# Performance work log

Measured on AMD Instinct MI355X. Metric: run time of the kernel, lower is better.

Reference implementation:

```python
import jax, jax.numpy as jnp
import numpy as np

B, H, W = 8, 64, 64
EMBED, HEADS, HEAD_DIM = 768, 12, 64
FF = 3072
WS = 14  # window size
SCALE = HEAD_DIM ** -0.5
EPS = 1e-6


def setup_inputs() -> dict:
    key = jax.random.key(0)
    ks = jax.random.split(key, 8)
    def n(k, shp, s=0.02):
        return jax.random.normal(k, shp, jnp.float32) * s
    return {
        "x": jax.random.normal(ks[0], (B, H, W, EMBED), jnp.float32),
        "g1": jnp.ones((EMBED,), jnp.float32),
        "beta1": jnp.zeros((EMBED,), jnp.float32),
        "w_qkv": n(ks[1], (EMBED, 3 * EMBED)),
        "b_qkv": jnp.zeros((3 * EMBED,), jnp.float32),
        "w_proj": n(ks[2], (EMBED, EMBED)),
        "b_proj": jnp.zeros((EMBED,), jnp.float32),
        "rel_pos_h": n(ks[3], (2 * WS - 1, HEAD_DIM)),
        "rel_pos_w": n(ks[4], (2 * WS - 1, HEAD_DIM)),
        "g2": jnp.ones((EMBED,), jnp.float32),
        "beta2": jnp.zeros((EMBED,), jnp.float32),
        "w_fc1": n(ks[5], (EMBED, FF)),
        "b_fc1": jnp.zeros((FF,), jnp.float32),
        "w_fc2": n(ks[6], (FF, EMBED)),
        "b_fc2": jnp.zeros((EMBED,), jnp.float32),
    }


def layer_norm(x, g, b):
    m = jnp.mean(x, axis=-1, keepdims=True)
    v = jnp.mean(jnp.square(x - m), axis=-1, keepdims=True)
    return (x - m) * jax.lax.rsqrt(v + EPS) * g + b


def window_partition(x):
    b, h, w, c = x.shape
    ph, pw = (-h) % WS, (-w) % WS
    x = jnp.pad(x, ((0, 0), (0, ph), (0, pw), (0, 0)))
    hp, wp = h + ph, w + pw
    x = x.reshape(b, hp // WS, WS, wp // WS, WS, c)
    x = x.transpose(0, 1, 3, 2, 4, 5).reshape(-1, WS, WS, c)
    return x, (hp, wp)


def window_unpartition(win, pad_hw, hw):
    hp, wp = pad_hw
    h, w = hw
    b = win.shape[0] // ((hp // WS) * (wp // WS))
    x = win.reshape(b, hp // WS, wp // WS, WS, WS, -1)
    x = x.transpose(0, 1, 3, 2, 4, 5).reshape(b, hp, wp, -1)
    return x[:, :h, :w, :]


def attention(xw, w_qkv, b_qkv, w_proj, b_proj, rel_pos_h, rel_pos_w):
    bw, hs, ws_, c = xw.shape
    n = hs * ws_
    qkv = (xw.reshape(bw, n, c) @ w_qkv + b_qkv).reshape(bw, n, 3, HEADS, HEAD_DIM)
    q, k, v = jnp.moveaxis(qkv, 2, 0)            # each (bw, n, heads, hd)
    q = q.transpose(0, 2, 1, 3)                  # (bw, heads, n, hd)
    k = k.transpose(0, 2, 1, 3)
    v = v.transpose(0, 2, 1, 3)
    attn = jnp.einsum('bhnd,bhmd->bhnm', q * SCALE, k)
    # decomposed relative position bias (q unscaled, per torch reference)
    idx = jnp.arange(WS)[:, None] - jnp.arange(WS)[None, :] + (WS - 1)
    Rh = rel_pos_h[idx]                          # (ws, ws, hd)
    Rw = rel_pos_w[idx]
    r_q = q.reshape(bw, HEADS, WS, WS, HEAD_DIM)
    rel_h = jnp.einsum('bhpqd,pkd->bhpqk', r_q, Rh)
    rel_w = jnp.einsum('bhpqd,qkd->bhpqk', r_q, Rw)
    attn = attn.reshape(bw, HEADS, WS, WS, WS, WS)
    attn = attn + rel_h[..., :, None] + rel_w[..., None, :]
    attn = jax.nn.softmax(attn.reshape(bw, HEADS, n, n), axis=-1)
    out = jnp.einsum('bhnm,bhmd->bhnd', attn, v)
    out = out.transpose(0, 2, 1, 3).reshape(bw, hs, ws_, c)
    return out @ w_proj + b_proj


def reference(x, g1, beta1, w_qkv, b_qkv, w_proj, b_proj, rel_pos_h, rel_pos_w,
              g2, beta2, w_fc1, b_fc1, w_fc2, b_fc2):
    shortcut = x
    h = layer_norm(x, g1, beta1)
    win, pad_hw = window_partition(h)
    a = attention(win, w_qkv, b_qkv, w_proj, b_proj, rel_pos_h, rel_pos_w)
    a = window_unpartition(a, pad_hw, (x.shape[1], x.shape[2]))
    x = shortcut + a
    h2 = layer_norm(x, g2, beta2)
    mlp = jax.nn.gelu(h2 @ w_fc1 + b_fc1, approximate=False) @ w_fc2 + b_fc2
    return x + mlp
```

## Files before the change

kernel.cpp:

```cpp
#include <hip/hip_runtime.h>
#include <cstdint>


typedef unsigned short u16;
typedef __attribute__((ext_vector_type(8))) short short8;
typedef __attribute__((ext_vector_type(4))) float f32x4;

__device__ __forceinline__ u16 f2b(float f) {
    union { float f; unsigned int i; } x; x.f = f;
    unsigned int u = x.i;
    return (u16)((u + 0x7fffu + ((u >> 16) & 1u)) >> 16);
}
__device__ __forceinline__ float b2f(u16 u) {
    union { unsigned int i; float f; } x; x.i = ((unsigned int)u) << 16; return x.f;
}

__device__ __forceinline__ void gload16(const u16* g, u16* l) {
    __builtin_amdgcn_global_load_lds(
        (const __attribute__((address_space(1))) unsigned int*)g,
        (__attribute__((address_space(3))) unsigned int*)l, 16, 0, 0);
}

__device__ __forceinline__ int xcd_swz(int bid, int nwg) {
    int q = nwg >> 3, r = nwg & 7;
    int x = bid & 7, lo = bid >> 3;
    return (x < r ? x * (q + 1) : r * (q + 1) + (x - r) * q) + lo;
}

__global__ __launch_bounds__(256) void transpose_k(
    const float* __restrict__ in, u16* __restrict__ out, int R, int C)
{
    __shared__ float tile[32][33];
    int bpc = C >> 5;
    int r0 = (blockIdx.x / bpc) << 5;
    int c0 = (blockIdx.x % bpc) << 5;
    int lx = threadIdx.x & 31, ly = threadIdx.x >> 5;
#pragma unroll
    for (int s = 0; s < 32; s += 8)
        tile[ly + s][lx] = in[(size_t)(r0 + ly + s) * C + c0 + lx];
    __syncthreads();
#pragma unroll
    for (int s = 0; s < 32; s += 8)
        out[(size_t)(c0 + ly + s) * R + r0 + lx] = f2b(tile[lx][ly + s]);
}

__global__ __launch_bounds__(256) void ln_kernel(
    const float* __restrict__ in, const float* __restrict__ g,
    const float* __restrict__ beta, u16* __restrict__ out, int windowed,
    int row_base)
{
    __shared__ float sbuf[4];
    int tid = threadIdx.x;
    size_t orow = (size_t)blockIdx.x * 768;
    size_t irow;
    if (windowed) {
        int r = row_base + blockIdx.x;
        int win = r / 196, t = r % 196;
        int p = t / 14, q = t % 14;
        int b = win / 25, wt = win % 25;
        int i = (wt / 5) * 14 + p, j = (wt % 5) * 14 + q;
        if (i >= 64 || j >= 64) {
            out[orow + tid] = 0; out[orow + tid + 256] = 0; out[orow + tid + 512] = 0;
            return;
        }
        irow = (((size_t)b * 64 + i) * 64 + j) * 768;
    } else {
        irow = (size_t)blockIdx.x * 768;
    }
    float v0 = in[irow + tid];
    float v1 = in[irow + tid + 256];
    float v2 = in[irow + tid + 512];
    float s = v0 + v1 + v2;
#pragma unroll
    for (int off = 32; off; off >>= 1) s += __shfl_xor(s, off, 64);
    if ((tid & 63) == 0) sbuf[tid >> 6] = s;
    __syncthreads();
    float mean = (sbuf[0] + sbuf[1] + sbuf[2] + sbuf[3]) * (1.f / 768.f);
    __syncthreads();
    float d0 = v0 - mean, d1 = v1 - mean, d2 = v2 - mean;
    float sq = d0 * d0 + d1 * d1 + d2 * d2;
#pragma unroll
    for (int off = 32; off; off >>= 1) sq += __shfl_xor(sq, off, 64);
    if ((tid & 63) == 0) sbuf[tid >> 6] = sq;
    __syncthreads();
    float var = (sbuf[0] + sbuf[1] + sbuf[2] + sbuf[3]) * (1.f / 768.f);
    float rs = rsqrtf(var + 1e-6f);
    out[orow + tid]       = f2b(d0 * rs * g[tid]       + beta[tid]);
    out[orow + tid + 256] = f2b(d1 * rs * g[tid + 256] + beta[tid + 256]);
    out[orow + tid + 512] = f2b(d2 * rs * g[tid + 512] + beta[tid + 512]);
}


__device__ __forceinline__ void compute_tile(
    const u16* Ab, const u16* Bb, f32x4 (&acc)[4][4],
    int wr, int wc, int quad, int l16, int l7)
{
    short8 a_[4][2], b_[4][2];
#pragma unroll
    for (int m = 0; m < 4; m++)
#pragma unroll
        for (int ks = 0; ks < 2; ks++)
            a_[m][ks] = *(const short8*)(Ab + (wr * 64 + m * 16 + l16) * 64
                                            + ((((ks << 2) + quad) ^ l7) << 3));
#pragma unroll
    for (int n = 0; n < 4; n++)
#pragma unroll
        for (int ks = 0; ks < 2; ks++)
            b_[n][ks] = *(const short8*)(Bb + (wc * 64 + n * 16 + l16) * 64
                                            + ((((ks << 2) + quad) ^ l7) << 3));
    __builtin_amdgcn_s_setprio(1);
#pragma unroll
    for (int m = 0; m < 4; m++)
#pragma unroll
        for (int n = 0; n < 4; n++)
#pragma unroll
            for (int ks = 0; ks < 2; ks++)
                acc[m][n] = __builtin_amdgcn_mfma_f32_16x16x32_bf16(
                    a_[m][ks], b_[n][ks], acc[m][n], 0, 0, 0);
    __builtin_amdgcn_s_setprio(0);
}

template <int EPI>
__global__ __launch_bounds__(256) void gemm128(
    const u16* __restrict__ A, const u16* __restrict__ Bt,
    const float* __restrict__ bias, void* __restrict__ CoutV,
    const float* __restrict__ resid, int M, int N, int K, int row_base)
{
    __shared__ __align__(16) u16 As0[128 * 64];
    __shared__ __align__(16) u16 As1[128 * 64];
    __shared__ __align__(16) u16 Bs0[128 * 64];
    __shared__ __align__(16) u16 Bs1[128 * 64];

    const int tid = threadIdx.x;
    const int lane = tid & 63, wave = tid >> 6;
    const int wr = wave >> 1, wc = wave & 1;
    const int quad = lane >> 4, l16 = lane & 15, l7 = lane & 7;
    const int ntile = N / 128;
    const int swz = xcd_swz(blockIdx.x, gridDim.x);
    const int m0 = (swz / ntile) * 128;
    const int n0 = (swz % ntile) * 128;

    const int rl = lane >> 3;
    const int cl = ((lane & 7) ^ rl) << 3;
    int aoff[4], boff[4];
#pragma unroll
    for (int q = 0; q < 4; q++) {
        aoff[q] = (m0 + wave * 32 + q * 8 + rl) * K + cl;
        boff[q] = (n0 + wave * 32 + q * 8 + rl) * K + cl;
    }
    const int lws = wave * 32 * 64;

    f32x4 acc[4][4] = {};
    const int nth = K >> 7;

#pragma unroll
    for (int q = 0; q < 4; q++) {
        gload16(A  + aoff[q], As0 + lws + q * 512);
        gload16(Bt + boff[q], Bs0 + lws + q * 512);
    }

#pragma unroll 1
    for (int it = 0; it < nth; ++it) {
        __builtin_amdgcn_sched_barrier(0);
        __builtin_amdgcn_s_barrier();
        __builtin_amdgcn_sched_barrier(0);
        {
            const int k1 = (2 * it + 1) << 6;
#pragma unroll
            for (int q = 0; q < 4; q++) {
                gload16(A  + aoff[q] + k1, As1 + lws + q * 512);
                gload16(Bt + boff[q] + k1, Bs1 + lws + q * 512);
            }
        }
        __builtin_amdgcn_sched_barrier(0);
        asm volatile("s_waitcnt vmcnt(8)" ::: "memory");
        __builtin_amdgcn_sched_barrier(0);
        __builtin_amdgcn_s_barrier();
        __builtin_amdgcn_sched_barrier(0);
        compute_tile(As0, Bs0, acc, wr, wc, quad, l16, l7);

        __builtin_amdgcn_sched_barrier(0);
        __builtin_amdgcn_s_barrier();
        __builtin_amdgcn_sched_barrier(0);
        if (it + 1 < nth) {
            const int k2 = (2 * it + 2) << 6;
#pragma unroll
            for (int q = 0; q < 4; q++) {
                gload16(A  + aoff[q] + k2, As0 + lws + q * 512);
                gload16(Bt + boff[q] + k2, Bs0 + lws + q * 512);
            }
            __builtin_amdgcn_sched_barrier(0);
            asm volatile("s_waitcnt vmcnt(8)" ::: "memory");
        } else {
            __builtin_amdgcn_sched_barrier(0);
            asm volatile("s_waitcnt vmcnt(0)" ::: "memory");
        }
        __builtin_amdgcn_sched_barrier(0);
        __builtin_amdgcn_s_barrier();
        __builtin_amdgcn_sched_barrier(0);
        compute_tile(As1, Bs1, acc, wr, wc, quad, l16, l7);
    }

#pragma unroll
    for (int mi = 0; mi < 4; mi++) {
#pragma unroll
        for (int ni = 0; ni < 4; ni++) {
            const int gn = n0 + wc * 64 + ni * 16 + l16;
            const float bv = bias[gn];
#pragma unroll
            for (int r = 0; r < 4; r++) {
                const int row = m0 + wr * 64 + mi * 16 + quad * 4 + r;
                if (row >= M) continue;
                float v = acc[mi][ni][r] + bv;
                if (EPI == 0) {
                    ((u16*)CoutV)[(size_t)row * N + gn] = f2b(v);
                } else if (EPI == 1) {
                    int grow = row_base + row;
                    int win = grow / 196, t = grow % 196;
                    int p = t / 14, q = t % 14;
                    int b_ = win / 25, wt = win % 25;
                    int i = (wt / 5) * 14 + p, j = (wt % 5) * 14 + q;
                    if (i < 64 && j < 64) {
                        size_t idx = (((size_t)b_ * 64 + i) * 64 + j) * 768 + gn;
                        ((float*)CoutV)[idx] = resid[idx] + v;
                    }
                } else if (EPI == 2) {
                    float gl = 0.5f * v * (1.0f + erff(v * 0.70710678118654752f));
                    ((u16*)CoutV)[(size_t)row * N + gn] = f2b(gl);
                } else {
                    size_t idx = (size_t)(row_base + row) * 768 + gn;
                    ((float*)CoutV)[idx] = resid[idx] + v;
                }
            }
        }
    }
}

#define AT_W 72
#define PB_W 40

__global__ __launch_bounds__(256) void attn_mfma(
    const u16* __restrict__ qkv,
    const float* __restrict__ relh, const float* __restrict__ relw,
    u16* __restrict__ out)
{
    __shared__ __align__(16) u16 pbuf[4][32 * PB_W];
    __shared__ __align__(16) u16 Kc[64 * AT_W];
    __shared__ __align__(16) u16 Vt[64 * AT_W];
    u16* rel_ext = &pbuf[0][0];

    const int nwg = gridDim.x;
    const int swzb = xcd_swz(blockIdx.x, nwg);
    const int win = swzb / 24, rem = swzb % 24;
    const int head = rem >> 1, half = rem & 1;
    const int row0 = half * 128;
    const int tid = threadIdx.x, lane = tid & 63, wave = tid >> 6;
    const int quad = lane >> 4, l16 = lane & 15;
    const size_t base = (size_t)win * 196 * 2304 + (size_t)head * 64;

    short8 qf[2][2];
#pragma unroll
    for (int mi = 0; mi < 2; mi++) {
        int tok = row0 + wave * 32 + mi * 16 + l16;
        int rt = tok < 196 ? tok : 195;
        const u16* qp = qkv + base + (size_t)rt * 2304 + quad * 8;
        qf[mi][0] = *(const short8*)(qp);
        qf[mi][1] = *(const short8*)(qp + 32);
    }

    for (int e = tid; e < 64 * 64; e += 256) {
        int rr = e >> 6, cc = e & 63;
        float v = 0.f;
        if (rr < 27)      v = 8.f * relh[rr * 64 + cc];
        else if (rr < 54) v = 8.f * relw[(rr - 27) * 64 + cc];
        Kc[rr * AT_W + cc] = f2b(v);
    }
    if (tid < 128) {
        u16* rp = rel_ext + tid * 32;
        uint4 z = make_uint4(0u, 0u, 0u, 0u);
        *(uint4*)(rp) = z; *(uint4*)(rp + 8) = z;
        *(uint4*)(rp + 16) = z; *(uint4*)(rp + 24) = z;
        rp[31] = f2b(-1e30f);
    }
    __syncthreads();

#pragma unroll
    for (int cb = 0; cb < 2; cb++) {
#pragma unroll
        for (int nt = 0; nt < 2; nt++) {
            const u16* kp_ = Kc + (cb * 32 + nt * 16 + l16) * AT_W + quad * 8;
            short8 b0 = *(const short8*)(kp_);
            short8 b1 = *(const short8*)(kp_ + 32);
            int i = cb * 32 + nt * 16 + l16;
#pragma unroll
            for (int mi = 0; mi < 2; mi++) {
                f32x4 c = {};
                c = __builtin_amdgcn_mfma_f32_16x16x32_bf16(qf[mi][0], b0, c, 0, 0, 0);
                c = __builtin_amdgcn_mfma_f32_16x16x32_bf16(qf[mi][1], b1, c, 0, 0, 0);
#pragma unroll
                for (int r = 0; r < 4; r++) {
                    int row = wave * 32 + mi * 16 + quad * 4 + r;
                    int grow = row0 + row;
                    int rowB = grow < 196 ? grow : 195;
                    int p = rowB / 14, qq = rowB % 14;
                    if (i < 27) {
                        int t = p + 13 - i;
                        if (t >= 0 && t < 14) rel_ext[row * 32 + t] = f2b(c[r]);
                    } else if (i < 54) {
                        int t = qq + 13 - (i - 27);
                        if (t >= 0 && t < 14) rel_ext[row * 32 + 14 + t] = f2b(c[r]);
                    }
                }
            }
        }
    }
    short8 qe[2];
#pragma unroll
    for (int mi = 0; mi < 2; mi++)
        qe[mi] = *(const short8*)(rel_ext + (wave * 32 + mi * 16 + l16) * 32 + quad * 8);

    f32x4 acc[2][4] = {};
    float ml_[2][4], ll_[2][4];
#pragma unroll
    for (int mi = 0; mi < 2; mi++)
#pragma unroll
        for (int r = 0; r < 4; r++) { ml_[mi][r] = -1e30f; ll_[mi][r] = 0.f; }

#pragma unroll 1
    for (int c = 0; c < 4; c++) {
        const int kbase = c * 64;
        __syncthreads();
        {
            int key = tid >> 2;
            int cg  = (tid & 3) << 4;
            int gk = kbase + key;
            uint4 k0 = make_uint4(0u,0u,0u,0u), k1 = k0, v0 = k0, v1 = k0;
            if (gk < 196) {
                const u16* kp_ = qkv + base + 768  + (size_t)gk * 2304 + cg;
                const u16* vp_ = qkv + base + 1536 + (size_t)gk * 2304 + cg;
                k0 = *(const uint4*)(kp_); k1 = *(const uint4*)(kp_ + 8);
                v0 = *(const uint4*)(vp_); v1 = *(const uint4*)(vp_ + 8);
            }
            *(uint4*)(Kc + key * AT_W + cg)     = k0;
            *(uint4*)(Kc + key * AT_W + cg + 8) = k1;
            union { uint4 u; u16 h[8]; } a, b; a.u = v0; b.u = v1;
#pragma unroll
            for (int i = 0; i < 8; i++) Vt[(cg + i) * AT_W + key] = a.h[i];
#pragma unroll
            for (int i = 0; i < 8; i++) Vt[(cg + 8 + i) * AT_W + key] = b.h[i];
        }
        __syncthreads();

        short8 bo[4];
        {
            const u16 one = 0x3F80;
#pragma unroll
            for (int nt = 0; nt < 4; nt++) {
                int key = kbase + nt * 16 + l16;
                int inval = key >= 196;
                int kp = key / 14, kq = key - kp * 14;
                union { short8 s; u16 h[8]; } u;
#pragma unroll
                for (int j = 0; j < 8; j++) {
                    int t = quad * 8 + j;
                    u16 v = 0;
                    if (!inval && t == kp) v = one;
                    if (!inval && t >= 14 && (t - 14) == kq) v = one;
                    if (inval && t == 31) v = one;
                    u.h[j] = v;
                }
                bo[nt] = u.s;
            }
        }

        f32x4 s23[2][2];
#pragma unroll
        for (int mi = 0; mi < 2; mi++) {
            f32x4 s[4];
            __builtin_amdgcn_s_setprio(1);
#pragma unroll
            for (int nt = 0; nt < 4; nt++) {
                const u16* kp_ = Kc + (nt * 16 + l16) * AT_W + quad * 8;
                short8 kf0 = *(const short8*)(kp_);
                short8 kf1 = *(const short8*)(kp_ + 32);
                f32x4 t = {};
                t = __builtin_amdgcn_mfma_f32_16x16x32_bf16(qf[mi][0], kf0, t, 0, 0, 0);
                t = __builtin_amdgcn_mfma_f32_16x16x32_bf16(qf[mi][1], kf1, t, 0, 0, 0);
                t = __builtin_amdgcn_mfma_f32_16x16x32_bf16(qe[mi],    bo[nt], t, 0, 0, 0);
                s[nt] = t * 0.125f;
            }
            __builtin_amdgcn_s_setprio(0);
#pragma unroll
            for (int r = 0; r < 4; r++) {
                float mx = fmaxf(fmaxf(s[0][r], s[1][r]), fmaxf(s[2][r], s[3][r]));
#pragma unroll
                for (int off = 8; off; off >>= 1) mx = fmaxf(mx, __shfl_xor(mx, off, 16));
                float mo = ml_[mi][r];
                float mn = fmaxf(mo, mx);
                float alpha = __expf(mo - mn);
                ml_[mi][r] = mn;
                float p0 = __expf(s[0][r] - mn), p1 = __expf(s[1][r] - mn);
                float p2 = __expf(s[2][r] - mn), p3 = __expf(s[3][r] - mn);
                float ps = (p0 + p1) + (p2 + p3);
#pragma unroll
                for (int off = 8; off; off >>= 1) ps += __shfl_xor(ps, off, 16);
                ll_[mi][r] = ll_[mi][r] * alpha + ps;
#pragma unroll
                for (int ni = 0; ni < 4; ni++) acc[mi][ni][r] *= alpha;
                s[0][r] = p0; s[1][r] = p1; s[2][r] = p2; s[3][r] = p3;
            }
#pragma unroll
            for (int nt = 0; nt < 2; nt++)
#pragma unroll
                for (int r = 0; r < 4; r++)
                    pbuf[wave][(mi * 16 + quad * 4 + r) * PB_W + nt * 16 + l16] = f2b(s[nt][r]);
            s23[mi][0] = s[2]; s23[mi][1] = s[3];
        }

        __builtin_amdgcn_s_setprio(1);
#pragma unroll
        for (int mi = 0; mi < 2; mi++) {
            short8 pf = *(const short8*)(pbuf[wave] + (mi * 16 + l16) * PB_W + quad * 8);
#pragma unroll
            for (int ni = 0; ni < 4; ni++) {
                short8 vfn = *(const short8*)(Vt + (ni * 16 + l16) * AT_W + quad * 8);
                acc[mi][ni] = __builtin_amdgcn_mfma_f32_16x16x32_bf16(pf, vfn, acc[mi][ni], 0, 0, 0);
            }
        }
        __builtin_amdgcn_s_setprio(0);
#pragma unroll
        for (int mi = 0; mi < 2; mi++)
#pragma unroll
            for (int h = 0; h < 2; h++)
#pragma unroll
                for (int r = 0; r < 4; r++)
                    pbuf[wave][(mi * 16 + quad * 4 + r) * PB_W + h * 16 + l16] = f2b(s23[mi][h][r]);
        __builtin_amdgcn_s_setprio(1);
#pragma unroll
        for (int mi = 0; mi < 2; mi++) {
            short8 pf = *(const short8*)(pbuf[wave] + (mi * 16 + l16) * PB_W + quad * 8);
#pragma unroll
            for (int ni = 0; ni < 4; ni++) {
                short8 vfn = *(const short8*)(Vt + (ni * 16 + l16) * AT_W + 32 + quad * 8);
                acc[mi][ni] = __builtin_amdgcn_mfma_f32_16x16x32_bf16(pf, vfn, acc[mi][ni], 0, 0, 0);
            }
        }
        __builtin_amdgcn_s_setprio(0);
    }

#pragma unroll
    for (int mi = 0; mi < 2; mi++)
#pragma unroll
        for (int r = 0; r < 4; r++) {
            int tok = row0 + wave * 32 + mi * 16 + quad * 4 + r;
            if (tok < 196) {
                float inv = 1.f / ll_[mi][r];
                size_t ob = (size_t)(win * 196 + tok) * 768 + head * 64;
#pragma unroll
                for (int ni = 0; ni < 4; ni++)
                    out[ob + ni * 16 + l16] = f2b(acc[mi][ni][r] * inv);
            }
        }
}

extern "C" void kernel_launch(void* const* d_in, const int* in_sizes, int n_in,
                              void* d_out, int out_size, void* d_ws, size_t ws_size,
                              hipStream_t stream)
{
    const float* x      = (const float*)d_in[0];
    const float* g1     = (const float*)d_in[1];
    const float* beta1  = (const float*)d_in[2];
    const float* w_qkv  = (const float*)d_in[3];
    const float* b_qkv  = (const float*)d_in[4];
    const float* w_proj = (const float*)d_in[5];
    const float* b_proj = (const float*)d_in[6];
    const float* rph    = (const float*)d_in[7];
    const float* rpw    = (const float*)d_in[8];
    const float* g2     = (const float*)d_in[9];
    const float* beta2  = (const float*)d_in[10];
    const float* w_fc1  = (const float*)d_in[11];
    const float* b_fc1  = (const float*)d_in[12];
    const float* w_fc2  = (const float*)d_in[13];
    const float* b_fc2  = (const float*)d_in[14];
    float* out = (float*)d_out;

    const size_t WT = 14155776;
    size_t b1 = 0, b2 = 0;
    int nc = 0, mc = 0;
    auto fits = [&](int a, int m) -> bool {
        size_t rows = (size_t)(200 / a) * 196, toks = (size_t)32768 / m;
        size_t bb1 = rows * 768 * 2 >= toks * 768 * 2 ? rows * 768 * 2 : toks * 768 * 2;
        size_t bb2 = rows * 2304 * 2 >= toks * 3072 * 2 ? rows * 2304 * 2 : toks * 3072 * 2;
        if (WT + bb1 + bb2 <= ws_size) { b1 = bb1; b2 = bb2; nc = a; mc = m; return true; }
        return false;
    };
    if (!fits(1, 1) && !fits(1, 2) && !fits(2, 2) && !fits(2, 4) && !fits(4, 4))
        return;

    char* ws = (char*)d_ws;
    u16* wt0 = (u16*)ws;
    u16* wt1 = wt0 + 2304 * 768;
    u16* wt2 = wt1 + 768 * 768;
    u16* wt3 = wt2 + 3072 * 768;
    u16* buf1 = (u16*)(ws + WT);
    u16* buf2 = (u16*)(ws + WT + b1);

    dim3 blk(256);

    transpose_k<<<(768/32)*(2304/32), blk, 0, stream>>>(w_qkv,  wt0, 768, 2304);
    transpose_k<<<(768/32)*(768/32),  blk, 0, stream>>>(w_proj, wt1, 768, 768);
    transpose_k<<<(768/32)*(3072/32), blk, 0, stream>>>(w_fc1,  wt2, 768, 3072);
    transpose_k<<<(3072/32)*(768/32), blk, 0, stream>>>(w_fc2,  wt3, 3072, 768);

    {
        const int nw = 200 / nc, rows = nw * 196;
        const int mt = (rows + 127) / 128;
        for (int c = 0; c < nc; c++) {
            const int rb = c * rows;
            ln_kernel<<<rows, blk, 0, stream>>>(x, g1, beta1, buf1, 1, rb);
            gemm128<0><<<dim3(mt * (2304/128)), blk, 0, stream>>>(
                buf1, wt0, b_qkv, buf2, nullptr, rows, 2304, 768, 0);
            attn_mfma<<<nw * 24, blk, 0, stream>>>(buf2, rph, rpw, buf1);
            gemm128<1><<<dim3(mt * (768/128)), blk, 0, stream>>>(
                buf1, wt1, b_proj, out, x, rows, 768, 768, rb);
        }
    }

    {
        const int tk = 32768 / mc;
        const int mt2 = tk / 128;
        for (int c = 0; c < mc; c++) {
            const int rb = c * tk;
            ln_kernel<<<tk, blk, 0, stream>>>(
                out + (size_t)rb * 768, g2, beta2, buf1, 0, 0);
            gemm128<2><<<dim3(mt2 * (3072/128)), blk, 0, stream>>>(
                buf1, wt2, b_fc1, buf2, nullptr, tk, 3072, 768, 0);
            gemm128<3><<<dim3(mt2 * (768/128)), blk, 0, stream>>>(
                buf2, wt3, b_fc2, out, out, tk, 768, 3072, rb);
        }
    }
}
```

Baseline: 1.545 ms.

## Enlarge GEMM block tile to 256x256 with 8 waves per block

Replaces the 128x128 GEMM tile (4 waves, 256 threads) with a 256x256 tile computed by 8 waves in a 2x4 layout. Each wave now owns a 128x64 output sub-tile, reusing its B fragments across two A halves. LDS use doubles to 128KB of double-buffered tiles. The aim is higher arithmetic intensity and less global/LDS traffic per FLOP, at the cost of fewer blocks (worse tail on the N=768 GEMMs), one block per CU, and more accumulator registers.

```diff
diff --git a/kernel.cpp b/kernel.cpp
--- a/kernel.cpp
+++ b/kernel.cpp
@@ -91,54 +91,61 @@
 }
 
 
-__device__ __forceinline__ void compute_tile(
-    const u16* Ab, const u16* Bb, f32x4 (&acc)[4][4],
-    int wr, int wc, int quad, int l16, int l7)
+__device__ __forceinline__ short8 lds_frag256(const u16* base, int row, int ks,
+                                              int quad) {
+    return *(const short8*)(base + row * 64 + ((((ks << 2) + quad) ^ (row & 7)) << 3));
+}
+
+__device__ __forceinline__ void compute_tile256(
+    const u16* Ab, const u16* Bb, f32x4 (&acc)[8][4],
+    int wr, int wc, int quad, int l16)
 {
-    short8 a_[4][2], b_[4][2];
-#pragma unroll
-    for (int m = 0; m < 4; m++)
+    short8 b_[4][2];
+#pragma unroll
+    for (int n = 0; n < 4; n++)
 #pragma unroll
         for (int ks = 0; ks < 2; ks++)
-            a_[m][ks] = *(const short8*)(Ab + (wr * 64 + m * 16 + l16) * 64
-                                            + ((((ks << 2) + quad) ^ l7) << 3));
-#pragma unroll
-    for (int n = 0; n < 4; n++)
-#pragma unroll
-        for (int ks = 0; ks < 2; ks++)
-            b_[n][ks] = *(const short8*)(Bb + (wc * 64 + n * 16 + l16) * 64
-                                            + ((((ks << 2) + quad) ^ l7) << 3));
-    __builtin_amdgcn_s_setprio(1);
-#pragma unroll
-    for (int m = 0; m < 4; m++)
-#pragma unroll
-        for (int n = 0; n < 4; n++)
+            b_[n][ks] = lds_frag256(Bb, wc * 64 + n * 16 + l16, ks, quad);
+#pragma unroll
+    for (int mq = 0; mq < 2; mq++) {
+        short8 a_[4][2];
+#pragma unroll
+        for (int m = 0; m < 4; m++)
 #pragma unroll
             for (int ks = 0; ks < 2; ks++)
-                acc[m][n] = __builtin_amdgcn_mfma_f32_16x16x32_bf16(
-                    a_[m][ks], b_[n][ks], acc[m][n], 0, 0, 0);
-    __builtin_amdgcn_s_setprio(0);
+                a_[m][ks] = lds_frag256(Ab, wr * 128 + mq * 64 + m * 16 + l16, ks, quad);
+        __builtin_amdgcn_s_setprio(1);
+#pragma unroll
+        for (int m = 0; m < 4; m++)
+#pragma unroll
+            for (int n = 0; n < 4; n++)
+#pragma unroll
+                for (int ks = 0; ks < 2; ks++)
+                    acc[mq * 4 + m][n] = __builtin_amdgcn_mfma_f32_16x16x32_bf16(
+                        a_[m][ks], b_[n][ks], acc[mq * 4 + m][n], 0, 0, 0);
+        __builtin_amdgcn_s_setprio(0);
+    }
 }
 
 template <int EPI>
-__global__ __launch_bounds__(256) void gemm128(
+__global__ __launch_bounds__(512) void gemm256(
     const u16* __restrict__ A, const u16* __restrict__ Bt,
     const float* __restrict__ bias, void* __restrict__ CoutV,
     const float* __restrict__ resid, int M, int N, int K, int row_base)
 {
-    __shared__ __align__(16) u16 As0[128 * 64];
-    __shared__ __align__(16) u16 As1[128 * 64];
-    __shared__ __align__(16) u16 Bs0[128 * 64];
-    __shared__ __align__(16) u16 Bs1[128 * 64];
+    __shared__ __align__(16) u16 As0[256 * 64];
+    __shared__ __align__(16) u16 As1[256 * 64];
+    __shared__ __align__(16) u16 Bs0[256 * 64];
+    __shared__ __align__(16) u16 Bs1[256 * 64];
 
     const int tid = threadIdx.x;
     const int lane = tid & 63, wave = tid >> 6;
-    const int wr = wave >> 1, wc = wave & 1;
-    const int quad = lane >> 4, l16 = lane & 15, l7 = lane & 7;
-    const int ntile = N / 128;
+    const int wr = wave >> 2, wc = wave & 3;
+    const int quad = lane >> 4, l16 = lane & 15;
+    const int ntile = N / 256;
     const int swz = xcd_swz(blockIdx.x, gridDim.x);
-    const int m0 = (swz / ntile) * 128;
-    const int n0 = (swz % ntile) * 128;
+    const int m0 = (swz / ntile) * 256;
+    const int n0 = (swz % ntile) * 256;
 
     const int rl = lane >> 3;
     const int cl = ((lane & 7) ^ rl) << 3;
@@ -148,9 +155,9 @@
         aoff[q] = (m0 + wave * 32 + q * 8 + rl) * K + cl;
         boff[q] = (n0 + wave * 32 + q * 8 + rl) * K + cl;
     }
-    const int lws = wave * 32 * 64;
-
-    f32x4 acc[4][4] = {};
+    const int lws = wave * 2048;
+
+    f32x4 acc[8][4] = {};
     const int nth = K >> 7;
 
 #pragma unroll
@@ -177,7 +184,7 @@
         __builtin_amdgcn_sched_barrier(0);
         __builtin_amdgcn_s_barrier();
         __builtin_amdgcn_sched_barrier(0);
-        compute_tile(As0, Bs0, acc, wr, wc, quad, l16, l7);
+        compute_tile256(As0, Bs0, acc, wr, wc, quad, l16);
 
         __builtin_amdgcn_sched_barrier(0);
         __builtin_amdgcn_s_barrier();
@@ -198,18 +205,18 @@
         __builtin_amdgcn_sched_barrier(0);
         __builtin_amdgcn_s_barrier();
         __builtin_amdgcn_sched_barrier(0);
-        compute_tile(As1, Bs1, acc, wr, wc, quad, l16, l7);
-    }
-
-#pragma unroll
-    for (int mi = 0; mi < 4; mi++) {
+        compute_tile256(As1, Bs1, acc, wr, wc, quad, l16);
+    }
+
+#pragma unroll
+    for (int mi = 0; mi < 8; mi++) {
 #pragma unroll
         for (int ni = 0; ni < 4; ni++) {
             const int gn = n0 + wc * 64 + ni * 16 + l16;
             const float bv = bias[gn];
 #pragma unroll
             for (int r = 0; r < 4; r++) {
-                const int row = m0 + wr * 64 + mi * 16 + quad * 4 + r;
+                const int row = m0 + wr * 128 + mi * 16 + quad * 4 + r;
                 if (row >= M) continue;
                 float v = acc[mi][ni][r] + bv;
                 if (EPI == 0) {
@@ -505,7 +512,7 @@
     u16* buf1 = (u16*)(ws + WT);
     u16* buf2 = (u16*)(ws + WT + b1);
 
-    dim3 blk(256);
+    dim3 blk(256), blk5(512);
 
     transpose_k<<<(768/32)*(2304/32), blk, 0, stream>>>(w_qkv,  wt0, 768, 2304);
     transpose_k<<<(768/32)*(768/32),  blk, 0, stream>>>(w_proj, wt1, 768, 768);
@@ -514,28 +521,28 @@
 
     {
         const int nw = 200 / nc, rows = nw * 196;
-        const int mt = (rows + 127) / 128;
+        const int mt = (rows + 255) / 256;
         for (int c = 0; c < nc; c++) {
             const int rb = c * rows;
             ln_kernel<<<rows, blk, 0, stream>>>(x, g1, beta1, buf1, 1, rb);
-            gemm128<0><<<dim3(mt * (2304/128)), blk, 0, stream>>>(
+            gemm256<0><<<dim3(mt * (2304/256)), blk5, 0, stream>>>(
                 buf1, wt0, b_qkv, buf2, nullptr, rows, 2304, 768, 0);
             attn_mfma<<<nw * 24, blk, 0, stream>>>(buf2, rph, rpw, buf1);
-            gemm128<1><<<dim3(mt * (768/128)), blk, 0, stream>>>(
+            gemm256<1><<<dim3(mt * (768/256)), blk5, 0, stream>>>(
                 buf1, wt1, b_proj, out, x, rows, 768, 768, rb);
         }
     }
 
     {
         const int tk = 32768 / mc;
-        const int mt2 = tk / 128;
+        const int mt2 = (tk + 255) / 256;
         for (int c = 0; c < mc; c++) {
             const int rb = c * tk;
             ln_kernel<<<tk, blk, 0, stream>>>(
                 out + (size_t)rb * 768, g2, beta2, buf1, 0, 0);
-            gemm128<2><<<dim3(mt2 * (3072/128)), blk, 0, stream>>>(
+            gemm256<2><<<dim3(mt2 * (3072/256)), blk5, 0, stream>>>(
                 buf1, wt2, b_fc1, buf2, nullptr, tk, 3072, 768, 0);
-            gemm128<3><<<dim3(mt2 * (768/128)), blk, 0, stream>>>(
+            gemm256<3><<<dim3(mt2 * (768/256)), blk5, 0, stream>>>(
                 buf2, wt3, b_fc2, out, out, tk, 768, 3072, rb);
         }
     }
```

Result: no change. 1.560 ms (+0.9%).
